# Kernel tuning notes

Measured on AMD Instinct MI355X. Metric: run time of the kernel, lower is better.

Reference implementation:

```python
import jax, jax.numpy as jnp
import numpy as np

N, E, F_IN, HID, H, G = 50000, 800000, 128, 128, 4, 64
D = HID // H  # per-head dim = 32


def setup_inputs() -> dict:
    key = jax.random.key(0)
    ks = jax.random.split(key, 24)
    s = 0.05
    x = jax.random.normal(ks[0], (N, F_IN), dtype=jnp.float32)
    edge_index = jax.random.randint(ks[1], (2, E), 0, N, dtype=jnp.int64)
    batch = jnp.sort(jax.random.randint(ks[2], (N,), 0, G, dtype=jnp.int64))
    p = {}
    # layer 1: in F_IN -> H*D, layer 2: in HID -> H*D; each conv has q,k,v,skip linears (bias=True)
    names = ['Wq1', 'Wk1', 'Wv1', 'Ws1', 'Wq2', 'Wk2', 'Wv2', 'Ws2']
    dims = [(F_IN, HID)] * 4 + [(HID, HID)] * 4
    for i, (nm, dm) in enumerate(zip(names, dims)):
        p[nm] = jax.random.normal(ks[3 + 2 * i], dm, dtype=jnp.float32) * s
        p['b' + nm[1:]] = jax.random.normal(ks[4 + 2 * i], (dm[1],), dtype=jnp.float32) * s
    p['Wfc'] = jax.random.normal(ks[20], (HID, 1), dtype=jnp.float32) * s
    p['bfc'] = jax.random.normal(ks[21], (1,), dtype=jnp.float32) * s
    return {'x': x, 'edge_index': edge_index, 'batch': batch, **p}


def transformer_conv(x, edge_index, Wq, bq, Wk, bk, Wv, bv, Ws, bs):
    src, dst = edge_index[0], edge_index[1]  # messages flow src -> dst
    q = (x @ Wq + bq).reshape(-1, H, D)[dst]          # [E,H,D]
    k = (x @ Wk + bk).reshape(-1, H, D)[src]          # [E,H,D]
    v = (x @ Wv + bv).reshape(-1, H, D)[src]          # [E,H,D]
    logits = jnp.einsum('ehd,ehd->eh', q, k) / jnp.sqrt(jnp.float32(D))  # [E,H]
    m = jax.ops.segment_max(logits, dst, num_segments=N)                 # [N,H]
    e = jnp.exp(logits - m[dst])
    s = jax.ops.segment_sum(e, dst, num_segments=N)                      # [N,H]
    alpha = e / s[dst]
    agg = jax.ops.segment_sum(alpha[..., None] * v, dst, num_segments=N)  # [N,H,D]
    return agg.reshape(-1, HID) + (x @ Ws + bs)


def reference(x, edge_index, batch, Wq1, bq1, Wk1, bk1, Wv1, bv1, Ws1, bs1,
              Wq2, bq2, Wk2, bk2, Wv2, bv2, Ws2, bs2, Wfc, bfc):
    h = jax.nn.relu(transformer_conv(x, edge_index, Wq1, bq1, Wk1, bk1, Wv1, bv1, Ws1, bs1))
    h = jax.nn.relu(transformer_conv(h, edge_index, Wq2, bq2, Wk2, bk2, Wv2, bv2, Ws2, bs2))
    sums = jax.ops.segment_sum(h, batch, num_segments=G)                 # [G,HID]
    cnt = jax.ops.segment_sum(jnp.ones((h.shape[0],), h.dtype), batch, num_segments=G)
    pooled = sums / jnp.maximum(cnt, 1.0)[:, None]
    return (pooled @ Wfc + bfc).squeeze(-1)
```

## Files before the change

kernel.cpp:

```cpp
#include <hip/hip_runtime.h>
#include <hip/hip_bf16.h>
#include <math.h>

#define HID 128

typedef __attribute__((ext_vector_type(8))) short short8;
typedef __attribute__((ext_vector_type(4))) short short4v;
typedef __attribute__((ext_vector_type(4))) float f32x4;
typedef __attribute__((ext_vector_type(2))) float f32x2;
typedef __attribute__((ext_vector_type(4))) unsigned short ushort4v;
typedef __attribute__((ext_vector_type(2))) unsigned short ushort2v;

static inline size_t align256(size_t x){ return (x + 255) & ~(size_t)255; }

__device__ inline float bf2f(unsigned short h) {
  union { unsigned u; float f; } uf; uf.u = ((unsigned)h) << 16; return uf.f;
}
__device__ inline unsigned short f2bf(float f) {
  union { float f; unsigned u; } uf; uf.f = f;
  unsigned r = uf.u + 0x7fff + ((uf.u >> 16) & 1);
  return (unsigned short)(r >> 16);
}

__device__ inline float dpp_rsum16(float x) {
  int v;
  v = __builtin_amdgcn_update_dpp(0, __float_as_int(x), 0xB1, 0xF, 0xF, true);
  x += __int_as_float(v);
  v = __builtin_amdgcn_update_dpp(0, __float_as_int(x), 0x4E, 0xF, 0xF, true);
  x += __int_as_float(v);
  v = __builtin_amdgcn_update_dpp(0, __float_as_int(x), 0x124, 0xF, 0xF, true);
  x += __int_as_float(v);
  v = __builtin_amdgcn_update_dpp(0, __float_as_int(x), 0x128, 0xF, 0xF, true);
  x += __int_as_float(v);
  return x;
}

__global__ __launch_bounds__(256) void k_wprep(
    const float* W0, const float* W1, const float* W2, const float* W3,
    const float* W4, const float* W5, const float* W6, const float* W7,
    const float* b0, const float* b1, const float* b2, const float* b3,
    const float* b4, const float* b5, const float* b6, const float* b7,
    unsigned short* Wcat, float* Bcat)
{
  __shared__ float tl[32][33];
  const float* Ws[8] = {W0, W1, W2, W3, W4, W5, W6, W7};
  const float* bs[8] = {b0, b1, b2, b3, b4, b5, b6, b7};
  int m = blockIdx.x >> 4, tile = blockIdx.x & 15;
  int tr = (tile >> 2) * 32, tc = (tile & 3) * 32;
  int tx = threadIdx.x & 31, ty = threadIdx.x >> 5;
  const float* Wm = Ws[m];
  #pragma unroll
  for (int r = 0; r < 32; r += 8) tl[ty + r][tx] = Wm[(tr + ty + r) * 128 + tc + tx];
  __syncthreads();
  #pragma unroll
  for (int r = 0; r < 32; r += 8)
    Wcat[m * 16384 + (tc + ty + r) * 128 + tr + tx] = f2bf(tl[tx][ty + r]);
  if (tile == 0 && threadIdx.x < 128) Bcat[m * 128 + threadIdx.x] = bs[m][threadIdx.x];
}

__global__ void k_hist(const int* __restrict__ dst, int* __restrict__ deg, int e) {
  for (int i = blockIdx.x * blockDim.x + threadIdx.x; i < e; i += gridDim.x * blockDim.x)
    atomicAdd(&deg[dst[i]], 1);
}

__global__ void k_scan_a(const int* __restrict__ deg, int* __restrict__ rowptr,
                         int* __restrict__ bsum, int n) {
  __shared__ int tmp[512];
  int t = threadIdx.x, i = blockIdx.x * 512 + t;
  int v = (i < n) ? deg[i] : 0;
  tmp[t] = v;
  __syncthreads();
  for (int off = 1; off < 512; off <<= 1) {
    int u = (t >= off) ? tmp[t - off] : 0;
    __syncthreads();
    tmp[t] += u;
    __syncthreads();
  }
  if (i < n) rowptr[i] = tmp[t] - v;
  if (t == 511) bsum[blockIdx.x] = tmp[t];
}

__global__ void k_scan_b(int* bsum, int nb) {
  __shared__ int tmp[512];
  int t = threadIdx.x;
  int v = (t < nb) ? bsum[t] : 0;
  tmp[t] = v;
  __syncthreads();
  for (int off = 1; off < 512; off <<= 1) {
    int u = (t >= off) ? tmp[t - off] : 0;
    __syncthreads();
    tmp[t] += u;
    __syncthreads();
  }
  if (t < nb) bsum[t] = tmp[t] - v;
}

__global__ void k_scan_c(int* __restrict__ rowptr, int* __restrict__ cursor,
                         const int* __restrict__ bsum, int n, int e) {
  int i = blockIdx.x * 512 + threadIdx.x;
  if (i < n) { int v = rowptr[i] + bsum[blockIdx.x]; rowptr[i] = v; cursor[i] = v; }
  if (i == 0) rowptr[n] = e;
}

__global__ void k_scatter(const int* __restrict__ srcA, const int* __restrict__ dstA,
                          int* __restrict__ cursor, int* __restrict__ csrc, int e) {
  for (int i = blockIdx.x * blockDim.x + threadIdx.x; i < e; i += gridDim.x * blockDim.x) {
    int pos = atomicAdd(&cursor[dstA[i]], 1);
    csrc[pos] = srcA[i] << 9;
  }
}

template<int ABF16>
__global__ __launch_bounds__(256, 2) void k_qkvs(
    const void* __restrict__ Ain, const unsigned short* __restrict__ Wl,
    const float* __restrict__ Bl, unsigned short* __restrict__ Qb,
    unsigned short* __restrict__ KVb, float* __restrict__ Sb, int n)
{
  __shared__ unsigned short sA[64 * 128];
  __shared__ unsigned short sW[128 * 128];
  const int tid = threadIdx.x;
  const int rb = blockIdx.x * 64;

  if (ABF16) {
    const unsigned short* A = (const unsigned short*)Ain;
    #pragma unroll
    for (int it = 0; it < 4; ++it) {
      int q = tid + it * 256;
      int row = q >> 4, ch = q & 15;
      int gr = rb + row;
      short8 h = {0,0,0,0,0,0,0,0};
      if (gr < n) h = *reinterpret_cast<const short8*>(A + (size_t)gr * HID + ch * 8);
      *reinterpret_cast<short8*>(&sA[row * 128 + ((ch ^ (row & 7)) << 3)]) = h;
    }
  } else {
    const float* A = (const float*)Ain;
    #pragma unroll
    for (int it = 0; it < 8; ++it) {
      int q = tid + it * 256;
      int row = q >> 5, c4 = (q & 31) * 4;
      int gr = rb + row;
      f32x4 a = {0.f, 0.f, 0.f, 0.f};
      if (gr < n) a = *reinterpret_cast<const f32x4*>(A + (size_t)gr * HID + c4);
      short4v h;
      h.x = (short)f2bf(a.x); h.y = (short)f2bf(a.y);
      h.z = (short)f2bf(a.z); h.w = (short)f2bf(a.w);
      int eloff = row * 128 + (((c4 >> 3) ^ (row & 7)) << 3) + (c4 & 7);
      *reinterpret_cast<short4v*>(&sA[eloff]) = h;
    }
  }

  const int lane = tid & 63;
  const int wv = tid >> 6;

  auto stageW = [&](int y) {
    const unsigned short* Wy = Wl + (size_t)y * 16384;
    #pragma unroll
    for (int it = 0; it < 8; ++it) {
      int q = tid + it * 256;
      int c = q >> 4, ch = q & 15;
      short8 w = *reinterpret_cast<const short8*>(Wy + c * 128 + ch * 8);
      *reinterpret_cast<short8*>(&sW[c * 128 + ((ch ^ (c & 7)) << 3)]) = w;
    }
  };

  stageW(0);
  __syncthreads();

  short8 af[4];
  #pragma unroll
  for (int ks = 0; ks < 4; ++ks) {
    int ch = ks * 4 + (lane >> 4);
    int row = wv * 16 + (lane & 15);
    af[ks] = *reinterpret_cast<const short8*>(&sA[row * 128 + ((ch ^ (row & 7)) << 3)]);
  }

  f32x4 acc[8];
  auto compute = [&]() {
    #pragma unroll
    for (int mf = 0; mf < 8; ++mf) acc[mf] = (f32x4){0.f, 0.f, 0.f, 0.f};
    #pragma unroll
    for (int ks = 0; ks < 4; ++ks) {
      int ch = ks * 4 + (lane >> 4);
      short8 wf[8];
      #pragma unroll
      for (int mf = 0; mf < 8; ++mf) {
        int wc = mf * 16 + (lane & 15);
        wf[mf] = *reinterpret_cast<const short8*>(&sW[wc * 128 + ((ch ^ (wc & 7)) << 3)]);
      }
      #pragma unroll
      for (int mf = 0; mf < 8; ++mf)
        acc[mf] = __builtin_amdgcn_mfma_f32_16x16x32_bf16(wf[mf], af[ks], acc[mf], 0, 0, 0);
    }
  };

  const int gr = rb + wv * 16 + (lane & 15);
  const int cbase = (lane >> 4) << 2;

  compute();
  if (gr < n) {
    #pragma unroll
    for (int mf = 0; mf < 8; ++mf) {
      int c0 = mf * 16 + cbase;
      f32x4 b = *reinterpret_cast<const f32x4*>(Bl + 0 * 128 + c0);
      f32x4 v = acc[mf];
      short4v h;
      h.x = (short)f2bf(v.x + b.x); h.y = (short)f2bf(v.y + b.y);
      h.z = (short)f2bf(v.z + b.z); h.w = (short)f2bf(v.w + b.w);
      *reinterpret_cast<short4v*>(Qb + (size_t)gr * HID + c0) = h;
    }
  }

  __syncthreads();
  stageW(3);
  __syncthreads();
  compute();
  if (gr < n) {
    #pragma unroll
    for (int mf = 0; mf < 8; ++mf) {
      int c0 = mf * 16 + cbase;
      f32x4 b = *reinterpret_cast<const f32x4*>(Bl + 3 * 128 + c0);
      f32x4 v = acc[mf];
      v.x += b.x; v.y += b.y; v.z += b.z; v.w += b.w;
      *reinterpret_cast<f32x4*>(Sb + (size_t)gr * HID + c0) = v;
    }
  }

  __syncthreads();
  stageW(1);
  __syncthreads();
  compute();
  f32x4 kacc[8];
  #pragma unroll
  for (int mf = 0; mf < 8; ++mf) kacc[mf] = acc[mf];

  __syncthreads();
  stageW(2);
  __syncthreads();
  compute();
  if (gr < n) {
    #pragma unroll
    for (int mf = 0; mf < 8; ++mf) {
      int c0 = mf * 16 + cbase;
      f32x4 bk = *reinterpret_cast<const f32x4*>(Bl + 1 * 128 + c0);
      f32x4 bv = *reinterpret_cast<const f32x4*>(Bl + 2 * 128 + c0);
      f32x4 kv = kacc[mf], vv = acc[mf];
      short8 h;
      h[0] = (short)f2bf(kv.x + bk.x); h[1] = (short)f2bf(kv.y + bk.y);
      h[2] = (short)f2bf(vv.x + bv.x); h[3] = (short)f2bf(vv.y + bv.y);
      h[4] = (short)f2bf(kv.z + bk.z); h[5] = (short)f2bf(kv.w + bk.w);
      h[6] = (short)f2bf(vv.z + bv.z); h[7] = (short)f2bf(vv.w + bv.w);
      *reinterpret_cast<short8*>(KVb + (size_t)gr * 256 + 2 * c0) = h;
    }
  }
}

__global__ __launch_bounds__(256) void k_attn2(
    const unsigned short* __restrict__ Qb, const unsigned short* __restrict__ KVb,
    const float* __restrict__ Sb, const int* __restrict__ rowptr,
    const int* __restrict__ csrc, unsigned short* __restrict__ Hout, int n)
{
  int wid = blockIdx.x * 4 + (threadIdx.x >> 6);
  if (wid >= n) return;
  int lane = threadIdx.x & 63;
  ushort2v qv = *reinterpret_cast<const ushort2v*>(Qb + (size_t)wid * HID + 2 * lane);
  const float sc = 0.25503487f;
  float q0 = bf2f(qv.x) * sc, q1 = bf2f(qv.y) * sc;
  int e0 = rowptr[wid], deg = rowptr[wid + 1] - e0;
  const int* cp = csrc + e0;
  const char* kvb = (const char*)KVb;
  float m = -INFINITY, s = 0.f, a0 = 0.f, a1 = 0.f;

  auto LD = [&](int i) -> ushort4v {
    return *reinterpret_cast<const ushort4v*>(kvb + (unsigned)cp[i] + lane * 8);
  };
  auto proc = [&](ushort4v kv) {
    float d = q0 * bf2f(kv.x) + q1 * bf2f(kv.y);
    float lg = dpp_rsum16(d);
    if (!__all(lg <= m + 11.5f)) {
      float nm = fmaxf(m, lg);
      float cc = __builtin_amdgcn_exp2f(m - nm);
      s *= cc; a0 *= cc; a1 *= cc; m = nm;
    }
    float p = __builtin_amdgcn_exp2f(lg - m);
    s += p;
    a0 = fmaf(p, bf2f(kv.z), a0);
    a1 = fmaf(p, bf2f(kv.w), a1);
  };

  int nq = deg >> 2, r = deg & 3;
  if (nq) {
    ushort4v b0 = LD(0), b1 = LD(1), b2 = LD(2), b3 = LD(3);
    for (int q = 1; q < nq; ++q) {
      int base = q * 4;
      ushort4v n0 = LD(base), n1 = LD(base + 1), n2 = LD(base + 2), n3 = LD(base + 3);
      proc(b0); proc(b1); proc(b2); proc(b3);
      b0 = n0; b1 = n1; b2 = n2; b3 = n3;
    }
    int tb = nq * 4;
    ushort4v t0, t1, t2;
    if (r > 0) t0 = LD(tb);
    if (r > 1) t1 = LD(tb + 1);
    if (r > 2) t2 = LD(tb + 2);
    proc(b0); proc(b1); proc(b2); proc(b3);
    if (r > 0) proc(t0);
    if (r > 1) proc(t1);
    if (r > 2) proc(t2);
  } else {
    for (int i = 0; i < r; ++i) proc(LD(i));
  }

  float inv = (s > 0.f) ? 1.f / s : 0.f;
  f32x2 sv = *reinterpret_cast<const f32x2*>(Sb + (size_t)wid * HID + 2 * lane);
  ushort2v h;
  h.x = f2bf(fmaxf(a0 * inv + sv.x, 0.f));
  h.y = f2bf(fmaxf(a1 * inv + sv.y, 0.f));
  *reinterpret_cast<ushort2v*>(Hout + (size_t)wid * HID + 2 * lane) = h;
}

__global__ void k_pool(const unsigned short* __restrict__ Hin, const int* __restrict__ batch,
                       float* __restrict__ psum, float* __restrict__ pcnt, int n) {
  int t = threadIdx.x;
  int chunk = (n + gridDim.x - 1) / gridDim.x;
  int n0 = blockIdx.x * chunk, n1 = min(n, n0 + chunk);
  if (n0 >= n1) return;
  int curg = batch[n0];
  float acc = 0.f; int c = 0;
  for (int i = n0; i < n1; ++i) {
    int g = batch[i];
    if (g != curg) {
      atomicAdd(&psum[curg * HID + t], acc);
      if (t == 0) atomicAdd(&pcnt[curg], (float)c);
      acc = 0.f; c = 0; curg = g;
    }
    acc += bf2f(Hin[(size_t)i * HID + t]); ++c;
  }
  atomicAdd(&psum[curg * HID + t], acc);
  if (t == 0) atomicAdd(&pcnt[curg], (float)c);
}

__global__ void k_fc(const float* __restrict__ psum, const float* __restrict__ pcnt,
                     const float* __restrict__ Wfc, const float* __restrict__ bfc,
                     float* __restrict__ out) {
  __shared__ float red[2];
  int g = blockIdx.x, t = threadIdx.x;
  float v = psum[g * HID + t] * Wfc[t];
  #pragma unroll
  for (int off = 32; off >= 1; off >>= 1) v += __shfl_xor(v, off);
  if ((t & 63) == 0) red[t >> 6] = v;
  __syncthreads();
  if (t == 0) out[g] = (red[0] + red[1]) / fmaxf(pcnt[g], 1.f) + bfc[0];
}

extern "C" void kernel_launch(void* const* d_in, const int* in_sizes, int n_in,
                              void* d_out, int out_size, void* d_ws, size_t ws_size,
                              hipStream_t stream)
{
  const float* x   = (const float*)d_in[0];
  const int*   ei  = (const int*)d_in[1];
  const int*   bat = (const int*)d_in[2];
  const float *Wq1 = (const float*)d_in[3],  *bq1 = (const float*)d_in[4];
  const float *Wk1 = (const float*)d_in[5],  *bk1 = (const float*)d_in[6];
  const float *Wv1 = (const float*)d_in[7],  *bv1 = (const float*)d_in[8];
  const float *Ws1 = (const float*)d_in[9],  *bs1 = (const float*)d_in[10];
  const float *Wq2 = (const float*)d_in[11], *bq2 = (const float*)d_in[12];
  const float *Wk2 = (const float*)d_in[13], *bk2 = (const float*)d_in[14];
  const float *Wv2 = (const float*)d_in[15], *bv2 = (const float*)d_in[16];
  const float *Ws2 = (const float*)d_in[17], *bs2 = (const float*)d_in[18];
  const float *Wfc = (const float*)d_in[19], *bfc = (const float*)d_in[20];
  float* out = (float*)d_out;

  const int N = in_sizes[0] / HID;
  const int E = in_sizes[1] / 2;
  const int G = 64;

  char* p = (char*)d_ws;
  auto alloc = [&](size_t bytes) -> char* { char* r = p; p += align256(bytes); return r; };
  unsigned short* Qb  = (unsigned short*)alloc((size_t)N * HID * 2);
  unsigned short* KVb = (unsigned short*)alloc((size_t)N * 256 * 2);
  float* Sb   = (float*)alloc((size_t)N * HID * 4);
  unsigned short* Hb  = (unsigned short*)alloc((size_t)N * HID * 2);
  unsigned short* H2b = (unsigned short*)alloc((size_t)N * HID * 2);
  unsigned short* Wcat = (unsigned short*)alloc((size_t)8 * 128 * 128 * 2);
  float* Bcat = (float*)alloc((size_t)8 * 128 * 4);
  int* rowptr = (int*)alloc((size_t)(N + 1) * sizeof(int));
  int* cursor = (int*)alloc((size_t)N * sizeof(int));
  int* deg    = (int*)alloc((size_t)N * sizeof(int));
  int* bsum   = (int*)alloc(4096);
  int* csrc   = (int*)alloc((size_t)E * sizeof(int));
  float* psum = (float*)alloc((size_t)G * HID * sizeof(float));
  float* pcnt = (float*)alloc((size_t)G * sizeof(float));

  const int* esrc = ei;
  const int* edst = ei + E;

  hipMemsetAsync(deg, 0, (size_t)N * sizeof(int), stream);
  hipMemsetAsync(psum, 0, (size_t)G * HID * sizeof(float), stream);
  hipMemsetAsync(pcnt, 0, (size_t)G * sizeof(float), stream);

  k_wprep<<<128, 256, 0, stream>>>(Wq1, Wk1, Wv1, Ws1, Wq2, Wk2, Wv2, Ws2,
                                   bq1, bk1, bv1, bs1, bq2, bk2, bv2, bs2, Wcat, Bcat);

  k_hist<<<512, 256, 0, stream>>>(edst, deg, E);
  int SB = (N + 511) / 512;
  k_scan_a<<<SB, 512, 0, stream>>>(deg, rowptr, bsum, N);
  k_scan_b<<<1, 512, 0, stream>>>(bsum, SB);
  k_scan_c<<<SB, 512, 0, stream>>>(rowptr, cursor, bsum, N, E);
  k_scatter<<<512, 256, 0, stream>>>(esrc, edst, cursor, csrc, E);

  int QB = (N + 63) / 64;
  k_qkvs<0><<<QB, 256, 0, stream>>>(x, Wcat, Bcat, Qb, KVb, Sb, N);
  k_attn2<<<(N + 3) / 4, 256, 0, stream>>>(Qb, KVb, Sb, rowptr, csrc, Hb, N);
  k_qkvs<1><<<QB, 256, 0, stream>>>(Hb, Wcat + 4 * 16384, Bcat + 512, Qb, KVb, Sb, N);
  k_attn2<<<(N + 3) / 4, 256, 0, stream>>>(Qb, KVb, Sb, rowptr, csrc, H2b, N);
  k_pool<<<1024, 128, 0, stream>>>(H2b, bat, psum, pcnt, N);
  k_fc<<<G, 128, 0, stream>>>(psum, pcnt, Wfc, bfc, out);
}
```

Measured before the change: 410.6 us.

## Merge preprocessing kernels, fuse scatter with first QKV GEMM, batch attention loads

Several small launches are folded together: the weight prep and degree histogram become one kernel, and the scan's middle pass is replaced by each block reducing the preceding block sums itself. The edge scatter is merged into the first QKV projection launch, and pooling plus the final FC become a single per-graph kernel that binary-searches the sorted batch vector instead of using atomics. The attention loop now loads four CSR offsets as one vector and does one max/rescale check per group of four edges. This targets launch overhead and serialization between tiny kernels. The cost is that pooling uses only 64 blocks, which may underuse the GPU, and scatter atomics now share the device with the GEMM blocks.

```diff
diff --git a/kernel.cpp b/kernel.cpp
--- a/kernel.cpp
+++ b/kernel.cpp
@@ -8,6 +8,7 @@
 typedef __attribute__((ext_vector_type(4))) short short4v;
 typedef __attribute__((ext_vector_type(4))) float f32x4;
 typedef __attribute__((ext_vector_type(2))) float f32x2;
+typedef __attribute__((ext_vector_type(4))) int int4v;
 typedef __attribute__((ext_vector_type(4))) unsigned short ushort4v;
 typedef __attribute__((ext_vector_type(2))) unsigned short ushort2v;
 
@@ -35,14 +36,20 @@
   return x;
 }
 
-__global__ __launch_bounds__(256) void k_wprep(
+__global__ __launch_bounds__(256) void k_prep(
     const float* W0, const float* W1, const float* W2, const float* W3,
     const float* W4, const float* W5, const float* W6, const float* W7,
     const float* b0, const float* b1, const float* b2, const float* b3,
     const float* b4, const float* b5, const float* b6, const float* b7,
-    unsigned short* Wcat, float* Bcat)
+    unsigned short* Wcat, float* Bcat,
+    const int* __restrict__ edst, int* __restrict__ deg, int e)
 {
   __shared__ float tl[32][33];
+  if (blockIdx.x >= 128) {
+    for (int i = (blockIdx.x - 128) * 256 + threadIdx.x; i < e; i += 512 * 256)
+      atomicAdd(&deg[edst[i]], 1);
+    return;
+  }
   const float* Ws[8] = {W0, W1, W2, W3, W4, W5, W6, W7};
   const float* bs[8] = {b0, b1, b2, b3, b4, b5, b6, b7};
   int m = blockIdx.x >> 4, tile = blockIdx.x & 15;
@@ -58,11 +65,6 @@
   if (tile == 0 && threadIdx.x < 128) Bcat[m * 128 + threadIdx.x] = bs[m][threadIdx.x];
 }
 
-__global__ void k_hist(const int* __restrict__ dst, int* __restrict__ deg, int e) {
-  for (int i = blockIdx.x * blockDim.x + threadIdx.x; i < e; i += gridDim.x * blockDim.x)
-    atomicAdd(&deg[dst[i]], 1);
-}
-
 __global__ void k_scan_a(const int* __restrict__ deg, int* __restrict__ rowptr,
                          int* __restrict__ bsum, int n) {
   __shared__ int tmp[512];
@@ -80,46 +82,38 @@
   if (t == 511) bsum[blockIdx.x] = tmp[t];
 }
 
-__global__ void k_scan_b(int* bsum, int nb) {
-  __shared__ int tmp[512];
+__global__ void k_scan_c(int* __restrict__ rowptr, int* __restrict__ cursor,
+                         const int* __restrict__ bsum, int n, int e, int nb) {
+  __shared__ int sred[8];
+  __shared__ int base_sh;
   int t = threadIdx.x;
-  int v = (t < nb) ? bsum[t] : 0;
-  tmp[t] = v;
-  __syncthreads();
-  for (int off = 1; off < 512; off <<= 1) {
-    int u = (t >= off) ? tmp[t - off] : 0;
-    __syncthreads();
-    tmp[t] += u;
-    __syncthreads();
-  }
-  if (t < nb) bsum[t] = tmp[t] - v;
-}
-
-__global__ void k_scan_c(int* __restrict__ rowptr, int* __restrict__ cursor,
-                         const int* __restrict__ bsum, int n, int e) {
-  int i = blockIdx.x * 512 + threadIdx.x;
-  if (i < n) { int v = rowptr[i] + bsum[blockIdx.x]; rowptr[i] = v; cursor[i] = v; }
+  int v = (t < nb && t < (int)blockIdx.x) ? bsum[t] : 0;
+  #pragma unroll
+  for (int off = 32; off >= 1; off >>= 1) v += __shfl_xor(v, off);
+  if ((t & 63) == 0) sred[t >> 6] = v;
+  __syncthreads();
+  if (t == 0) {
+    int b = 0;
+    #pragma unroll
+    for (int j = 0; j < 8; ++j) b += sred[j];
+    base_sh = b;
+  }
+  __syncthreads();
+  int base = base_sh;
+  int i = blockIdx.x * 512 + t;
+  if (i < n) { int val = rowptr[i] + base; rowptr[i] = val; cursor[i] = val; }
   if (i == 0) rowptr[n] = e;
 }
 
-__global__ void k_scatter(const int* __restrict__ srcA, const int* __restrict__ dstA,
-                          int* __restrict__ cursor, int* __restrict__ csrc, int e) {
-  for (int i = blockIdx.x * blockDim.x + threadIdx.x; i < e; i += gridDim.x * blockDim.x) {
-    int pos = atomicAdd(&cursor[dstA[i]], 1);
-    csrc[pos] = srcA[i] << 9;
-  }
-}
-
 template<int ABF16>
-__global__ __launch_bounds__(256, 2) void k_qkvs(
-    const void* __restrict__ Ain, const unsigned short* __restrict__ Wl,
+__device__ __forceinline__ void qkvs_body(
+    int bx, const void* __restrict__ Ain, const unsigned short* __restrict__ Wl,
     const float* __restrict__ Bl, unsigned short* __restrict__ Qb,
-    unsigned short* __restrict__ KVb, float* __restrict__ Sb, int n)
-{
-  __shared__ unsigned short sA[64 * 128];
-  __shared__ unsigned short sW[128 * 128];
+    unsigned short* __restrict__ KVb, float* __restrict__ Sb, int n,
+    unsigned short* sA, unsigned short* sW)
+{
   const int tid = threadIdx.x;
-  const int rb = blockIdx.x * 64;
+  const int rb = bx * 64;
 
   if (ABF16) {
     const unsigned short* A = (const unsigned short*)Ain;
@@ -254,6 +248,35 @@
   }
 }
 
+__global__ __launch_bounds__(256, 2) void k_scat_qkvs1(
+    const int* __restrict__ srcA, const int* __restrict__ dstA,
+    int* __restrict__ cursor, int* __restrict__ csrc, int e,
+    const void* __restrict__ Ain, const unsigned short* __restrict__ Wl,
+    const float* __restrict__ Bl, unsigned short* __restrict__ Qb,
+    unsigned short* __restrict__ KVb, float* __restrict__ Sb, int n)
+{
+  __shared__ unsigned short sA[64 * 128];
+  __shared__ unsigned short sW[128 * 128];
+  if (blockIdx.x < 512) {
+    for (int i = blockIdx.x * 256 + threadIdx.x; i < e; i += 512 * 256) {
+      int pos = atomicAdd(&cursor[dstA[i]], 1);
+      csrc[pos] = srcA[i] << 9;
+    }
+    return;
+  }
+  qkvs_body<0>(blockIdx.x - 512, Ain, Wl, Bl, Qb, KVb, Sb, n, sA, sW);
+}
+
+__global__ __launch_bounds__(256, 2) void k_qkvs2(
+    const void* __restrict__ Ain, const unsigned short* __restrict__ Wl,
+    const float* __restrict__ Bl, unsigned short* __restrict__ Qb,
+    unsigned short* __restrict__ KVb, float* __restrict__ Sb, int n)
+{
+  __shared__ unsigned short sA[64 * 128];
+  __shared__ unsigned short sW[128 * 128];
+  qkvs_body<1>(blockIdx.x, Ain, Wl, Bl, Qb, KVb, Sb, n, sA, sW);
+}
+
 __global__ __launch_bounds__(256) void k_attn2(
     const unsigned short* __restrict__ Qb, const unsigned short* __restrict__ KVb,
     const float* __restrict__ Sb, const int* __restrict__ rowptr,
@@ -267,13 +290,13 @@
   float q0 = bf2f(qv.x) * sc, q1 = bf2f(qv.y) * sc;
   int e0 = rowptr[wid], deg = rowptr[wid + 1] - e0;
   const int* cp = csrc + e0;
-  const char* kvb = (const char*)KVb;
+  const char* kvb = (const char*)KVb + lane * 8;
   float m = -INFINITY, s = 0.f, a0 = 0.f, a1 = 0.f;
 
-  auto LD = [&](int i) -> ushort4v {
-    return *reinterpret_cast<const ushort4v*>(kvb + (unsigned)cp[i] + lane * 8);
+  auto LDo = [&](int off) -> ushort4v {
+    return *reinterpret_cast<const ushort4v*>(kvb + (unsigned)off);
   };
-  auto proc = [&](ushort4v kv) {
+  auto proc1 = [&](ushort4v kv) {
     float d = q0 * bf2f(kv.x) + q1 * bf2f(kv.y);
     float lg = dpp_rsum16(d);
     if (!__all(lg <= m + 11.5f)) {
@@ -286,28 +309,42 @@
     a0 = fmaf(p, bf2f(kv.z), a0);
     a1 = fmaf(p, bf2f(kv.w), a1);
   };
+  auto proc4 = [&](ushort4v e0v, ushort4v e1v, ushort4v e2v, ushort4v e3v) {
+    float d0 = q0 * bf2f(e0v.x) + q1 * bf2f(e0v.y);
+    float d1 = q0 * bf2f(e1v.x) + q1 * bf2f(e1v.y);
+    float d2 = q0 * bf2f(e2v.x) + q1 * bf2f(e2v.y);
+    float d3 = q0 * bf2f(e3v.x) + q1 * bf2f(e3v.y);
+    float l0 = dpp_rsum16(d0), l1 = dpp_rsum16(d1);
+    float l2 = dpp_rsum16(d2), l3 = dpp_rsum16(d3);
+    float qm = fmaxf(fmaxf(l0, l1), fmaxf(l2, l3));
+    if (!__all(qm <= m + 11.5f)) {
+      float nm = fmaxf(m, qm);
+      float cc = __builtin_amdgcn_exp2f(m - nm);
+      s *= cc; a0 *= cc; a1 *= cc; m = nm;
+    }
+    float p0 = __builtin_amdgcn_exp2f(l0 - m);
+    float p1 = __builtin_amdgcn_exp2f(l1 - m);
+    float p2 = __builtin_amdgcn_exp2f(l2 - m);
+    float p3 = __builtin_amdgcn_exp2f(l3 - m);
+    s += (p0 + p1) + (p2 + p3);
+    a0 = fmaf(p3, bf2f(e3v.z), fmaf(p2, bf2f(e2v.z), fmaf(p1, bf2f(e1v.z), fmaf(p0, bf2f(e0v.z), a0))));
+    a1 = fmaf(p3, bf2f(e3v.w), fmaf(p2, bf2f(e2v.w), fmaf(p1, bf2f(e1v.w), fmaf(p0, bf2f(e0v.w), a1))));
+  };
 
   int nq = deg >> 2, r = deg & 3;
   if (nq) {
-    ushort4v b0 = LD(0), b1 = LD(1), b2 = LD(2), b3 = LD(3);
+    int4v o; __builtin_memcpy(&o, cp, 16);
+    ushort4v b0 = LDo(o.x), b1 = LDo(o.y), b2 = LDo(o.z), b3 = LDo(o.w);
     for (int q = 1; q < nq; ++q) {
-      int base = q * 4;
-      ushort4v n0 = LD(base), n1 = LD(base + 1), n2 = LD(base + 2), n3 = LD(base + 3);
-      proc(b0); proc(b1); proc(b2); proc(b3);
+      int4v no; __builtin_memcpy(&no, cp + 4 * q, 16);
+      ushort4v n0 = LDo(no.x), n1 = LDo(no.y), n2 = LDo(no.z), n3 = LDo(no.w);
+      proc4(b0, b1, b2, b3);
       b0 = n0; b1 = n1; b2 = n2; b3 = n3;
     }
-    int tb = nq * 4;
-    ushort4v t0, t1, t2;
-    if (r > 0) t0 = LD(tb);
-    if (r > 1) t1 = LD(tb + 1);
-    if (r > 2) t2 = LD(tb + 2);
-    proc(b0); proc(b1); proc(b2); proc(b3);
-    if (r > 0) proc(t0);
-    if (r > 1) proc(t1);
-    if (r > 2) proc(t2);
-  } else {
-    for (int i = 0; i < r; ++i) proc(LD(i));
-  }
+    proc4(b0, b1, b2, b3);
+  }
+  int tb = nq * 4;
+  for (int i = 0; i < r; ++i) proc1(LDo(cp[tb + i]));
 
   float inv = (s > 0.f) ? 1.f / s : 0.f;
   f32x2 sv = *reinterpret_cast<const f32x2*>(Sb + (size_t)wid * HID + 2 * lane);
@@ -317,38 +354,42 @@
   *reinterpret_cast<ushort2v*>(Hout + (size_t)wid * HID + 2 * lane) = h;
 }
 
-__global__ void k_pool(const unsigned short* __restrict__ Hin, const int* __restrict__ batch,
-                       float* __restrict__ psum, float* __restrict__ pcnt, int n) {
+__global__ __launch_bounds__(256) void k_poolfc(
+    const unsigned short* __restrict__ H, const int* __restrict__ batch,
+    const float* __restrict__ Wfc, const float* __restrict__ bfc,
+    float* __restrict__ out, int n)
+{
+  int g = blockIdx.x;
+  int lo = 0, hi = n;
+  while (lo < hi) { int mid = (lo + hi) >> 1; if (batch[mid] < g) lo = mid + 1; else hi = mid; }
+  int start = lo;
+  hi = n;
+  while (lo < hi) { int mid = (lo + hi) >> 1; if (batch[mid] < g + 1) lo = mid + 1; else hi = mid; }
+  int end = lo;
+
   int t = threadIdx.x;
-  int chunk = (n + gridDim.x - 1) / gridDim.x;
-  int n0 = blockIdx.x * chunk, n1 = min(n, n0 + chunk);
-  if (n0 >= n1) return;
-  int curg = batch[n0];
-  float acc = 0.f; int c = 0;
-  for (int i = n0; i < n1; ++i) {
-    int g = batch[i];
-    if (g != curg) {
-      atomicAdd(&psum[curg * HID + t], acc);
-      if (t == 0) atomicAdd(&pcnt[curg], (float)c);
-      acc = 0.f; c = 0; curg = g;
-    }
-    acc += bf2f(Hin[(size_t)i * HID + t]); ++c;
-  }
-  atomicAdd(&psum[curg * HID + t], acc);
-  if (t == 0) atomicAdd(&pcnt[curg], (float)c);
-}
-
-__global__ void k_fc(const float* __restrict__ psum, const float* __restrict__ pcnt,
-                     const float* __restrict__ Wfc, const float* __restrict__ bfc,
-                     float* __restrict__ out) {
-  __shared__ float red[2];
-  int g = blockIdx.x, t = threadIdx.x;
-  float v = psum[g * HID + t] * Wfc[t];
+  int col = t & 127, rr = t >> 7;
+  float a0 = 0.f, a1 = 0.f, a2 = 0.f, a3 = 0.f;
+  int i = start + rr;
+  for (; i + 6 < end; i += 8) {
+    a0 += bf2f(H[(size_t)i * HID + col]);
+    a1 += bf2f(H[(size_t)(i + 2) * HID + col]);
+    a2 += bf2f(H[(size_t)(i + 4) * HID + col]);
+    a3 += bf2f(H[(size_t)(i + 6) * HID + col]);
+  }
+  for (; i < end; i += 2) a0 += bf2f(H[(size_t)i * HID + col]);
+  float v = ((a0 + a1) + (a2 + a3)) * Wfc[col];
+
+  __shared__ float red[4];
   #pragma unroll
   for (int off = 32; off >= 1; off >>= 1) v += __shfl_xor(v, off);
   if ((t & 63) == 0) red[t >> 6] = v;
   __syncthreads();
-  if (t == 0) out[g] = (red[0] + red[1]) / fmaxf(pcnt[g], 1.f) + bfc[0];
+  if (t == 0) {
+    float tot = (red[0] + red[1]) + (red[2] + red[3]);
+    float cnt = (float)(end - start);
+    out[g] = tot / fmaxf(cnt, 1.f) + bfc[0];
+  }
 }
 
 extern "C" void kernel_launch(void* const* d_in, const int* in_sizes, int n_in,
@@ -387,31 +428,24 @@
   int* deg    = (int*)alloc((size_t)N * sizeof(int));
   int* bsum   = (int*)alloc(4096);
   int* csrc   = (int*)alloc((size_t)E * sizeof(int));
-  float* psum = (float*)alloc((size_t)G * HID * sizeof(float));
-  float* pcnt = (float*)alloc((size_t)G * sizeof(float));
 
   const int* esrc = ei;
   const int* edst = ei + E;
 
   hipMemsetAsync(deg, 0, (size_t)N * sizeof(int), stream);
-  hipMemsetAsync(psum, 0, (size_t)G * HID * sizeof(float), stream);
-  hipMemsetAsync(pcnt, 0, (size_t)G * sizeof(float), stream);
-
-  k_wprep<<<128, 256, 0, stream>>>(Wq1, Wk1, Wv1, Ws1, Wq2, Wk2, Wv2, Ws2,
-                                   bq1, bk1, bv1, bs1, bq2, bk2, bv2, bs2, Wcat, Bcat);
-
-  k_hist<<<512, 256, 0, stream>>>(edst, deg, E);
+
+  k_prep<<<640, 256, 0, stream>>>(Wq1, Wk1, Wv1, Ws1, Wq2, Wk2, Wv2, Ws2,
+                                  bq1, bk1, bv1, bs1, bq2, bk2, bv2, bs2,
+                                  Wcat, Bcat, edst, deg, E);
   int SB = (N + 511) / 512;
   k_scan_a<<<SB, 512, 0, stream>>>(deg, rowptr, bsum, N);
-  k_scan_b<<<1, 512, 0, stream>>>(bsum, SB);
-  k_scan_c<<<SB, 512, 0, stream>>>(rowptr, cursor, bsum, N, E);
-  k_scatter<<<512, 256, 0, stream>>>(esrc, edst, cursor, csrc, E);
+  k_scan_c<<<SB, 512, 0, stream>>>(rowptr, cursor, bsum, N, E, SB);
 
   int QB = (N + 63) / 64;
-  k_qkvs<0><<<QB, 256, 0, stream>>>(x, Wcat, Bcat, Qb, KVb, Sb, N);
+  k_scat_qkvs1<<<512 + QB, 256, 0, stream>>>(esrc, edst, cursor, csrc, E,
+                                             x, Wcat, Bcat, Qb, KVb, Sb, N);
   k_attn2<<<(N + 3) / 4, 256, 0, stream>>>(Qb, KVb, Sb, rowptr, csrc, Hb, N);
-  k_qkvs<1><<<QB, 256, 0, stream>>>(Hb, Wcat + 4 * 16384, Bcat + 512, Qb, KVb, Sb, N);
+  k_qkvs2<<<QB, 256, 0, stream>>>(Hb, Wcat + 4 * 16384, Bcat + 512, Qb, KVb, Sb, N);
   k_attn2<<<(N + 3) / 4, 256, 0, stream>>>(Qb, KVb, Sb, rowptr, csrc, H2b, N);
-  k_pool<<<1024, 128, 0, stream>>>(H2b, bat, psum, pcnt, N);
-  k_fc<<<G, 128, 0, stream>>>(psum, pcnt, Wfc, bfc, out);
-}
+  k_poolfc<<<G, 256, 0, stream>>>(H2b, bat, Wfc, bfc, out, N);
+}
```

Result: faster. 398.3 us (-3.0%).
